# Kernel optimization log

Hardware: AMD Instinct MI355X
Metric: run time of the kernel (lower is better)

The kernel has to match this reference:

```python
import jax, jax.numpy as jnp
import numpy as np
import math

NUM_FILTERS = 128
SAMPLE_RATE = 16000
N_FFT = 2048
FREQ_MIN, FREQ_MAX = 20.0, 8000.0


def setup_inputs() -> dict:
    key = jax.random.key(0)
    B, FB, T = 32, N_FFT // 2 + 1, 2000
    spectrum = jax.random.normal(key, (B, FB, T), dtype=jnp.float32)
    # mel-scale init of center frequencies (in FFT-bin units), as in __init__
    mel_min = 2595.0 * math.log10(1.0 + FREQ_MIN / 700.0)
    mel_max = 2595.0 * math.log10(1.0 + FREQ_MAX / 700.0)
    mel_points = jnp.linspace(mel_min, mel_max, NUM_FILTERS, dtype=jnp.float32)
    freq_points = 700.0 * (10.0 ** (mel_points / 2595.0) - 1.0)
    center_freqs = freq_points * N_FFT / SAMPLE_RATE  # [F]
    bandwidths = jnp.full((NUM_FILTERS,), N_FFT / NUM_FILTERS / 4.0, dtype=jnp.float32)
    filter_shapes = jnp.ones((NUM_FILTERS, 2), dtype=jnp.float32)
    return {"spectrum": spectrum, "center_freqs": center_freqs,
            "bandwidths": bandwidths, "filter_shapes": filter_shapes}


def _build_filterbank(center_freqs, bandwidths, filter_shapes, freq_bins):
    # Vectorized over all filters: [F, freq_bins]
    freqs = jnp.arange(freq_bins, dtype=jnp.float32)[None, :]        # [1, K]
    center = center_freqs[:, None]                                    # [F, 1]
    bw = (jax.nn.softplus(bandwidths) + 0.001)[:, None]               # [F, 1]
    slopes = jax.nn.softplus(filter_shapes) + 0.1                     # [F, 2]
    left_edge = center - bw * slopes[:, 0:1]
    right_edge = center + bw * slopes[:, 1:2]
    rise = (freqs >= left_edge) & (freqs <= center)
    fall = (freqs > center) & (freqs <= right_edge)
    resp = jnp.where(rise, (freqs - left_edge) / (center - left_edge + 1e-8), 0.0)
    resp = jnp.where(fall, 1.0 - (freqs - center) / (right_edge - center + 1e-8), resp)
    return resp  # [F, K]


def reference(spectrum, center_freqs, bandwidths, filter_shapes):
    B, K, T = spectrum.shape
    F = center_freqs.shape[0]
    filterbank = _build_filterbank(center_freqs, bandwidths, filter_shapes, K)
    # [F, K] x [B, K, T] -> [B, F, T]
    filtered = jnp.einsum('fk,bkt->bft', filterbank, spectrum)
    # Faithful to original: reshape [B, F, T] -> [F, B, T], then permute(1,2,0) -> [B, T, F]
    filtered = filtered.reshape(F, B, T)
    return jnp.transpose(filtered, (1, 2, 0))
```

## Files before the change

### kernel.cpp

```cpp
#include <hip/hip_runtime.h>

#define K_BINS 1025
#define T_LEN  2000
#define NF     128
#define TQ     500

__device__ __forceinline__ float softplusf(float x) {
    return fmaxf(x, 0.0f) + log1pf(expf(-fabsf(x)));
}

__global__ __launch_bounds__(1024) void fb_fused(
        const float* __restrict__ spec,
        const float* __restrict__ cf,
        const float* __restrict__ bwv,
        const float* __restrict__ fs,
        float*       __restrict__ out) {
    const int q    = blockIdx.x;
    const int B    = blockIdx.y;
    const int th   = blockIdx.z;
    const int tid  = threadIdx.x;
    const int lane = tid & 63;
    const int wid  = tid >> 6;
    const int w    = wid >> 2;
    const int p    = wid & 3;
    const int bp   = 4 * q + p;
    const int t0   = TQ * th;

    float icl[4], irc[4], Af[4], Bf[4];
    int   klo[4], khi[4];
#pragma unroll
    for (int i = 0; i < 4; ++i) {
        const int f = 4 * B + 32 * w + i;
        float c  = cf[f];
        float bw = softplusf(bwv[f]) + 0.001f;
        float s0 = softplusf(fs[2 * f])     + 0.1f;
        float s1 = softplusf(fs[2 * f + 1]) + 0.1f;
        float left  = c - bw * s0;
        float right = c + bw * s1;
        icl[i] = 1.0f / (c - left + 1e-8f);
        irc[i] = 1.0f / (right - c + 1e-8f);
        Af[i]  = left * icl[i];
        Bf[i]  = fmaf(c, irc[i], 1.0f);
        klo[i] = max(0, (int)ceilf(left));
        khi[i] = min(K_BINS - 1, (int)floorf(right));
    }

    int rs[4], re[4], nr = 0;
    {
        int cs = klo[0], ce = khi[0];
#pragma unroll
        for (int i = 1; i < 4; ++i) {
            if (klo[i] <= ce + 1) ce = max(ce, khi[i]);
            else { rs[nr] = cs; re[nr] = ce; ++nr; cs = klo[i]; ce = khi[i]; }
        }
        rs[nr] = cs; re[nr] = ce; ++nr;
    }

    float4 acc[4][2];
#pragma unroll
    for (int i = 0; i < 4; ++i) {
        acc[i][0] = make_float4(0.f, 0.f, 0.f, 0.f);
        acc[i][1] = make_float4(0.f, 0.f, 0.f, 0.f);
    }

    const float4* base4 =
        (const float4*)(spec + (size_t)bp * (K_BINS * (size_t)T_LEN) + t0);
    const bool ok1 = (64 + lane) < (TQ / 4);

    int rcur = 0;
    int kcur = rs[0];
    float4 v0 = base4[(size_t)kcur * 500 + lane];
    float4 v1 = make_float4(0.f, 0.f, 0.f, 0.f);
    if (ok1) v1 = base4[(size_t)kcur * 500 + 64 + lane];

    while (kcur >= 0) {
        int knext, rnext = rcur;
        if (kcur + 1 <= re[rcur])      knext = kcur + 1;
        else if (rcur + 1 < nr)        { rnext = rcur + 1; knext = rs[rnext]; }
        else                           knext = -1;

        float4 n0, n1;
        if (knext >= 0) {
            const float4* np = base4 + (size_t)knext * 500;
            n0 = np[lane];
            if (ok1) n1 = np[64 + lane];
        }

        float fk = (float)kcur;
#pragma unroll
        for (int i = 0; i < 4; ++i) {
            float rise = fmaf(fk, icl[i], -Af[i]);
            float fall = fmaf(-fk, irc[i], Bf[i]);
            float wg   = fmaxf(0.0f, fminf(rise, fall));
            acc[i][0].x = fmaf(wg, v0.x, acc[i][0].x);
            acc[i][0].y = fmaf(wg, v0.y, acc[i][0].y);
            acc[i][0].z = fmaf(wg, v0.z, acc[i][0].z);
            acc[i][0].w = fmaf(wg, v0.w, acc[i][0].w);
            acc[i][1].x = fmaf(wg, v1.x, acc[i][1].x);
            acc[i][1].y = fmaf(wg, v1.y, acc[i][1].y);
            acc[i][1].z = fmaf(wg, v1.z, acc[i][1].z);
            acc[i][1].w = fmaf(wg, v1.w, acc[i][1].w);
        }
        v0 = n0; v1 = n1;
        kcur = knext; rcur = rnext;
    }

    __shared__ float tile[512][17];
#pragma unroll
    for (int i = 0; i < 4; ++i) {
        __syncthreads();
        {
            const int col = 4 * p + w;
            const int r0  = 4 * lane;
#pragma unroll
            for (int r = 0; r < 4; ++r)
                tile[r0 + r][col] = (&acc[i][0].x)[r];
            if (ok1) {
                const int r1 = 256 + 4 * lane;
#pragma unroll
                for (int r = 0; r < 4; ++r)
                    tile[r1 + r][col] = (&acc[i][1].x)[r];
            }
        }
        __syncthreads();
        const int b2 = 4 * B + i;
        const int c4 = tid & 3;
#pragma unroll
        for (int rr = 0; rr < 2; ++rr) {
            int tl = 256 * rr + (tid >> 2);
            if (tl < TQ) {
                float4 v = make_float4(tile[tl][4 * c4 + 0], tile[tl][4 * c4 + 1],
                                       tile[tl][4 * c4 + 2], tile[tl][4 * c4 + 3]);
                *reinterpret_cast<float4*>(
                    out + ((size_t)b2 * T_LEN + t0 + tl) * NF + 16 * q + 4 * c4) = v;
            }
        }
    }
}

extern "C" void kernel_launch(void* const* d_in, const int* in_sizes, int n_in,
                              void* d_out, int out_size, void* d_ws, size_t ws_size,
                              hipStream_t stream) {
    const float* spec = (const float*)d_in[0];
    const float* cf   = (const float*)d_in[1];
    const float* bwv  = (const float*)d_in[2];
    const float* fs   = (const float*)d_in[3];
    float* out = (float*)d_out;

    fb_fused<<<dim3(8, 8, 4), 1024, 0, stream>>>(spec, cf, bwv, fs, out);
}
```

Measured before the change: 61.91 us.

## Rebalance filter-band work per warp and narrow time tiles to one float4 per lane

Each warp now handles two filter groups, a band and its mirror (3-j, 7-Bp), so wide high-frequency filters pair with narrow low-frequency ones and per-warp k-loop lengths even out. The time axis is split into 8 tiles of 256 (last one 208), so each lane loads a single float4 per bin instead of two. The grid becomes 8x4x8 with the same block count. The aim is to cut the load imbalance across warps, where the slowest warp sets block time, at the cost of two sequential k-loops per warp and more output-tile passes through shared memory.

Result: slower. 69.07 us (+11.6%).

```diff
diff --git a/kernel.cpp b/kernel.cpp
--- a/kernel.cpp
+++ b/kernel.cpp
@@ -3,7 +3,6 @@
 #define K_BINS 1025
 #define T_LEN  2000
 #define NF     128
-#define TQ     500
 
 __device__ __forceinline__ float softplusf(float x) {
     return fmaxf(x, 0.0f) + log1pf(expf(-fabsf(x)));
@@ -16,123 +15,115 @@
         const float* __restrict__ fs,
         float*       __restrict__ out) {
     const int q    = blockIdx.x;
-    const int B    = blockIdx.y;
+    const int Bp   = blockIdx.y;
     const int th   = blockIdx.z;
     const int tid  = threadIdx.x;
     const int lane = tid & 63;
     const int wid  = tid >> 6;
-    const int w    = wid >> 2;
+    const int j    = wid >> 2;
     const int p    = wid & 3;
     const int bp   = 4 * q + p;
-    const int t0   = TQ * th;
-
-    float icl[4], irc[4], Af[4], Bf[4];
-    int   klo[4], khi[4];
-#pragma unroll
-    for (int i = 0; i < 4; ++i) {
-        const int f = 4 * B + 32 * w + i;
-        float c  = cf[f];
-        float bw = softplusf(bwv[f]) + 0.001f;
-        float s0 = softplusf(fs[2 * f])     + 0.1f;
-        float s1 = softplusf(fs[2 * f + 1]) + 0.1f;
-        float left  = c - bw * s0;
-        float right = c + bw * s1;
-        icl[i] = 1.0f / (c - left + 1e-8f);
-        irc[i] = 1.0f / (right - c + 1e-8f);
-        Af[i]  = left * icl[i];
-        Bf[i]  = fmaf(c, irc[i], 1.0f);
-        klo[i] = max(0, (int)ceilf(left));
-        khi[i] = min(K_BINS - 1, (int)floorf(right));
-    }
-
-    int rs[4], re[4], nr = 0;
-    {
-        int cs = klo[0], ce = khi[0];
-#pragma unroll
-        for (int i = 1; i < 4; ++i) {
-            if (klo[i] <= ce + 1) ce = max(ce, khi[i]);
-            else { rs[nr] = cs; re[nr] = ce; ++nr; cs = klo[i]; ce = khi[i]; }
-        }
-        rs[nr] = cs; re[nr] = ce; ++nr;
-    }
-
-    float4 acc[4][2];
-#pragma unroll
-    for (int i = 0; i < 4; ++i) {
-        acc[i][0] = make_float4(0.f, 0.f, 0.f, 0.f);
-        acc[i][1] = make_float4(0.f, 0.f, 0.f, 0.f);
-    }
+    const int t0   = 256 * th;
+    const int Lt   = (th < 7) ? 256 : 208;
+    const int Lq   = Lt >> 2;
+    const int li   = min(lane, Lq - 1);
 
     const float4* base4 =
         (const float4*)(spec + (size_t)bp * (K_BINS * (size_t)T_LEN) + t0);
-    const bool ok1 = (64 + lane) < (TQ / 4);
 
-    int rcur = 0;
-    int kcur = rs[0];
-    float4 v0 = base4[(size_t)kcur * 500 + lane];
-    float4 v1 = make_float4(0.f, 0.f, 0.f, 0.f);
-    if (ok1) v1 = base4[(size_t)kcur * 500 + 64 + lane];
+    float4 acc[2][4];
+#pragma unroll
+    for (int s = 0; s < 2; ++s)
+#pragma unroll
+        for (int i = 0; i < 4; ++i) acc[s][i] = make_float4(0.f, 0.f, 0.f, 0.f);
 
-    while (kcur >= 0) {
-        int knext, rnext = rcur;
-        if (kcur + 1 <= re[rcur])      knext = kcur + 1;
-        else if (rcur + 1 < nr)        { rnext = rcur + 1; knext = rs[rnext]; }
-        else                           knext = -1;
+#pragma unroll
+    for (int s = 0; s < 2; ++s) {
+        const int band  = s ? 3 - j : j;
+        const int Bq    = s ? 7 - Bp : Bp;
+        const int fbase = 4 * Bq + 32 * band;
 
-        float4 n0, n1;
-        if (knext >= 0) {
-            const float4* np = base4 + (size_t)knext * 500;
-            n0 = np[lane];
-            if (ok1) n1 = np[64 + lane];
+        float icl[4], irc[4], Af[4], Bf[4];
+        int   klo[4], khi[4];
+#pragma unroll
+        for (int i = 0; i < 4; ++i) {
+            const int f = fbase + i;
+            float c  = cf[f];
+            float bw = softplusf(bwv[f]) + 0.001f;
+            float s0 = softplusf(fs[2 * f])     + 0.1f;
+            float s1 = softplusf(fs[2 * f + 1]) + 0.1f;
+            float left  = c - bw * s0;
+            float right = c + bw * s1;
+            icl[i] = 1.0f / (c - left + 1e-8f);
+            irc[i] = 1.0f / (right - c + 1e-8f);
+            Af[i]  = left * icl[i];
+            Bf[i]  = fmaf(c, irc[i], 1.0f);
+            klo[i] = max(0, (int)ceilf(left));
+            khi[i] = min(K_BINS - 1, (int)floorf(right));
         }
 
-        float fk = (float)kcur;
+        int rs[4], re[4], nr = 0;
+        {
+            int cs = klo[0], ce = khi[0];
+#pragma unroll
+            for (int i = 1; i < 4; ++i) {
+                if (klo[i] <= ce + 1) ce = max(ce, khi[i]);
+                else { rs[nr] = cs; re[nr] = ce; ++nr; cs = klo[i]; ce = khi[i]; }
+            }
+            rs[nr] = cs; re[nr] = ce; ++nr;
+        }
+
+        int rcur = 0;
+        int kcur = rs[0];
+        float4 v = base4[(size_t)kcur * 500 + li];
+        while (kcur >= 0) {
+            int knext, rnext = rcur;
+            if (kcur + 1 <= re[rcur])      knext = kcur + 1;
+            else if (rcur + 1 < nr)        { rnext = rcur + 1; knext = rs[rnext]; }
+            else                           knext = -1;
+
+            float4 n;
+            if (knext >= 0) n = base4[(size_t)knext * 500 + li];
+
+            float fk = (float)kcur;
+#pragma unroll
+            for (int i = 0; i < 4; ++i) {
+                float rise = fmaf(fk, icl[i], -Af[i]);
+                float fall = fmaf(-fk, irc[i], Bf[i]);
+                float wg   = fmaxf(0.0f, fminf(rise, fall));
+                acc[s][i].x = fmaf(wg, v.x, acc[s][i].x);
+                acc[s][i].y = fmaf(wg, v.y, acc[s][i].y);
+                acc[s][i].z = fmaf(wg, v.z, acc[s][i].z);
+                acc[s][i].w = fmaf(wg, v.w, acc[s][i].w);
+            }
+            v = n; kcur = knext; rcur = rnext;
+        }
+    }
+
+    __shared__ float tile[256][17];
+#pragma unroll
+    for (int s = 0; s < 2; ++s) {
+        const int band = s ? 3 - j : j;
+        const int Bq   = s ? 7 - Bp : Bp;
+        const int col  = 4 * p + band;
 #pragma unroll
         for (int i = 0; i < 4; ++i) {
-            float rise = fmaf(fk, icl[i], -Af[i]);
-            float fall = fmaf(-fk, irc[i], Bf[i]);
-            float wg   = fmaxf(0.0f, fminf(rise, fall));
-            acc[i][0].x = fmaf(wg, v0.x, acc[i][0].x);
-            acc[i][0].y = fmaf(wg, v0.y, acc[i][0].y);
-            acc[i][0].z = fmaf(wg, v0.z, acc[i][0].z);
-            acc[i][0].w = fmaf(wg, v0.w, acc[i][0].w);
-            acc[i][1].x = fmaf(wg, v1.x, acc[i][1].x);
-            acc[i][1].y = fmaf(wg, v1.y, acc[i][1].y);
-            acc[i][1].z = fmaf(wg, v1.z, acc[i][1].z);
-            acc[i][1].w = fmaf(wg, v1.w, acc[i][1].w);
-        }
-        v0 = n0; v1 = n1;
-        kcur = knext; rcur = rnext;
-    }
-
-    __shared__ float tile[512][17];
-#pragma unroll
-    for (int i = 0; i < 4; ++i) {
-        __syncthreads();
-        {
-            const int col = 4 * p + w;
-            const int r0  = 4 * lane;
-#pragma unroll
-            for (int r = 0; r < 4; ++r)
-                tile[r0 + r][col] = (&acc[i][0].x)[r];
-            if (ok1) {
-                const int r1 = 256 + 4 * lane;
+            __syncthreads();
+            if (lane < Lq) {
+                const int rb = 4 * lane;
 #pragma unroll
                 for (int r = 0; r < 4; ++r)
-                    tile[r1 + r][col] = (&acc[i][1].x)[r];
+                    tile[rb + r][col] = (&acc[s][i].x)[r];
             }
-        }
-        __syncthreads();
-        const int b2 = 4 * B + i;
-        const int c4 = tid & 3;
-#pragma unroll
-        for (int rr = 0; rr < 2; ++rr) {
-            int tl = 256 * rr + (tid >> 2);
-            if (tl < TQ) {
-                float4 v = make_float4(tile[tl][4 * c4 + 0], tile[tl][4 * c4 + 1],
-                                       tile[tl][4 * c4 + 2], tile[tl][4 * c4 + 3]);
+            __syncthreads();
+            const int b2  = 4 * Bq + i;
+            const int row = tid >> 2;
+            const int c4  = tid & 3;
+            if (row < Lt) {
+                float4 v4 = make_float4(tile[row][4 * c4 + 0], tile[row][4 * c4 + 1],
+                                        tile[row][4 * c4 + 2], tile[row][4 * c4 + 3]);
                 *reinterpret_cast<float4*>(
-                    out + ((size_t)b2 * T_LEN + t0 + tl) * NF + 16 * q + 4 * c4) = v;
+                    out + ((size_t)b2 * T_LEN + t0 + row) * NF + 16 * q + 4 * c4) = v4;
             }
         }
     }
@@ -147,5 +138,5 @@
     const float* fs   = (const float*)d_in[3];
     float* out = (float*)d_out;
 
-    fb_fused<<<dim3(8, 8, 4), 1024, 0, stream>>>(spec, cf, bwv, fs, out);
+    fb_fused<<<dim3(8, 4, 8), 1024, 0, stream>>>(spec, cf, bwv, fs, out);
 }
```

## Fold four filter groups per wave and deepen row prefetch to three

Applied to the files above, without the earlier changes.

Blocks shrink from 1024 to 256 threads. Each wave now loops over four filter groups, which it previously shared with three other waves, and keeps all 4x4x2 float4 accumulators in registers. Inside each group, a three-slot rotating prefetch keeps several spectrum rows in flight ahead of the FMAs. The aim is more memory-level parallelism per wave, but register pressure rises sharply, occupancy per block drops, and the grid of 256 blocks leaves fewer waves in total to hide latency.

New measurement: 130.7 us. 2.11x slower.

```diff
diff --git a/kernel.cpp b/kernel.cpp
--- a/kernel.cpp
+++ b/kernel.cpp
@@ -4,12 +4,13 @@
 #define T_LEN  2000
 #define NF     128
 #define TQ     500
+#define ROWQ   500
 
 __device__ __forceinline__ float softplusf(float x) {
     return fmaxf(x, 0.0f) + log1pf(expf(-fabsf(x)));
 }
 
-__global__ __launch_bounds__(1024) void fb_fused(
+__global__ __launch_bounds__(256) void fb_fused(
         const float* __restrict__ spec,
         const float* __restrict__ cf,
         const float* __restrict__ bwv,
@@ -20,114 +21,132 @@
     const int th   = blockIdx.z;
     const int tid  = threadIdx.x;
     const int lane = tid & 63;
-    const int wid  = tid >> 6;
-    const int w    = wid >> 2;
-    const int p    = wid & 3;
+    const int p    = tid >> 6;
     const int bp   = 4 * q + p;
     const int t0   = TQ * th;
-
-    float icl[4], irc[4], Af[4], Bf[4];
-    int   klo[4], khi[4];
-#pragma unroll
-    for (int i = 0; i < 4; ++i) {
-        const int f = 4 * B + 32 * w + i;
-        float c  = cf[f];
-        float bw = softplusf(bwv[f]) + 0.001f;
-        float s0 = softplusf(fs[2 * f])     + 0.1f;
-        float s1 = softplusf(fs[2 * f + 1]) + 0.1f;
-        float left  = c - bw * s0;
-        float right = c + bw * s1;
-        icl[i] = 1.0f / (c - left + 1e-8f);
-        irc[i] = 1.0f / (right - c + 1e-8f);
-        Af[i]  = left * icl[i];
-        Bf[i]  = fmaf(c, irc[i], 1.0f);
-        klo[i] = max(0, (int)ceilf(left));
-        khi[i] = min(K_BINS - 1, (int)floorf(right));
-    }
-
-    int rs[4], re[4], nr = 0;
-    {
-        int cs = klo[0], ce = khi[0];
-#pragma unroll
-        for (int i = 1; i < 4; ++i) {
-            if (klo[i] <= ce + 1) ce = max(ce, khi[i]);
-            else { rs[nr] = cs; re[nr] = ce; ++nr; cs = klo[i]; ce = khi[i]; }
-        }
-        rs[nr] = cs; re[nr] = ce; ++nr;
-    }
-
-    float4 acc[4][2];
-#pragma unroll
-    for (int i = 0; i < 4; ++i) {
-        acc[i][0] = make_float4(0.f, 0.f, 0.f, 0.f);
-        acc[i][1] = make_float4(0.f, 0.f, 0.f, 0.f);
-    }
+    const bool ok1 = lane < (TQ / 4 - 64);
 
     const float4* base4 =
         (const float4*)(spec + (size_t)bp * (K_BINS * (size_t)T_LEN) + t0);
-    const bool ok1 = (64 + lane) < (TQ / 4);
 
-    int rcur = 0;
-    int kcur = rs[0];
-    float4 v0 = base4[(size_t)kcur * 500 + lane];
-    float4 v1 = make_float4(0.f, 0.f, 0.f, 0.f);
-    if (ok1) v1 = base4[(size_t)kcur * 500 + 64 + lane];
-
-    while (kcur >= 0) {
-        int knext, rnext = rcur;
-        if (kcur + 1 <= re[rcur])      knext = kcur + 1;
-        else if (rcur + 1 < nr)        { rnext = rcur + 1; knext = rs[rnext]; }
-        else                           knext = -1;
-
-        float4 n0, n1;
-        if (knext >= 0) {
-            const float4* np = base4 + (size_t)knext * 500;
-            n0 = np[lane];
-            if (ok1) n1 = np[64 + lane];
+    float4 acc[4][4][2];
+#pragma unroll
+    for (int w = 0; w < 4; ++w)
+#pragma unroll
+        for (int i = 0; i < 4; ++i) {
+            acc[w][i][0] = make_float4(0.f, 0.f, 0.f, 0.f);
+            acc[w][i][1] = make_float4(0.f, 0.f, 0.f, 0.f);
         }
 
-        float fk = (float)kcur;
+#pragma unroll
+    for (int w = 0; w < 4; ++w) {
+        float icl[4], mirc[4], mAf[4], Bf[4];
+        int   klo[4], khi[4];
 #pragma unroll
         for (int i = 0; i < 4; ++i) {
-            float rise = fmaf(fk, icl[i], -Af[i]);
-            float fall = fmaf(-fk, irc[i], Bf[i]);
-            float wg   = fmaxf(0.0f, fminf(rise, fall));
-            acc[i][0].x = fmaf(wg, v0.x, acc[i][0].x);
-            acc[i][0].y = fmaf(wg, v0.y, acc[i][0].y);
-            acc[i][0].z = fmaf(wg, v0.z, acc[i][0].z);
-            acc[i][0].w = fmaf(wg, v0.w, acc[i][0].w);
-            acc[i][1].x = fmaf(wg, v1.x, acc[i][1].x);
-            acc[i][1].y = fmaf(wg, v1.y, acc[i][1].y);
-            acc[i][1].z = fmaf(wg, v1.z, acc[i][1].z);
-            acc[i][1].w = fmaf(wg, v1.w, acc[i][1].w);
+            const int f = 4 * B + 32 * w + i;
+            float c  = cf[f];
+            float bw = softplusf(bwv[f]) + 0.001f;
+            float s0 = softplusf(fs[2 * f])     + 0.1f;
+            float s1 = softplusf(fs[2 * f + 1]) + 0.1f;
+            float left  = c - bw * s0;
+            float right = c + bw * s1;
+            float ic = 1.0f / (c - left + 1e-8f);
+            float ir = 1.0f / (right - c + 1e-8f);
+            icl[i]  = ic;
+            mirc[i] = -ir;
+            mAf[i]  = -left * ic;
+            Bf[i]   = fmaf(c, ir, 1.0f);
+            klo[i] = max(0, (int)ceilf(left));
+            khi[i] = min(K_BINS - 1, (int)floorf(right));
         }
-        v0 = n0; v1 = n1;
-        kcur = knext; rcur = rnext;
+
+        int rs[4], re[4], nr = 0;
+        {
+            int cs = klo[0], ce = khi[0];
+#pragma unroll
+            for (int i = 1; i < 4; ++i) {
+                if (klo[i] <= ce + 1) ce = max(ce, khi[i]);
+                else { rs[nr] = cs; re[nr] = ce; ++nr; cs = klo[i]; ce = khi[i]; }
+            }
+            rs[nr] = cs; re[nr] = ce; ++nr;
+        }
+
+        int rF = 0, kF = rs[0];
+        auto advance = [&]() {
+            if (kF + 1 <= re[rF]) ++kF;
+            else if (rF + 1 < nr) { ++rF; kF = rs[rF]; }
+            else kF = -1;
+        };
+
+#define LOADROW(d0, d1)                                                   \
+        { const float4* rp_ = base4 + (size_t)kF * ROWQ;                  \
+          d0 = rp_[lane]; if (ok1) d1 = rp_[64 + lane]; }
+
+#define COMPUTE(kk, v0, v1)                                               \
+        { float fk_ = (float)(kk);                                        \
+          _Pragma("unroll")                                               \
+          for (int i = 0; i < 4; ++i) {                                   \
+              float rise_ = fmaf(fk_, icl[i],  mAf[i]);                   \
+              float fall_ = fmaf(fk_, mirc[i], Bf[i]);                    \
+              float wg_   = fmaxf(0.0f, fminf(rise_, fall_));             \
+              acc[w][i][0].x = fmaf(wg_, v0.x, acc[w][i][0].x);           \
+              acc[w][i][0].y = fmaf(wg_, v0.y, acc[w][i][0].y);           \
+              acc[w][i][0].z = fmaf(wg_, v0.z, acc[w][i][0].z);           \
+              acc[w][i][0].w = fmaf(wg_, v0.w, acc[w][i][0].w);           \
+              acc[w][i][1].x = fmaf(wg_, v1.x, acc[w][i][1].x);           \
+              acc[w][i][1].y = fmaf(wg_, v1.y, acc[w][i][1].y);           \
+              acc[w][i][1].z = fmaf(wg_, v1.z, acc[w][i][1].z);           \
+              acc[w][i][1].w = fmaf(wg_, v1.w, acc[w][i][1].w);           \
+          } }
+
+#define STEP(S0, S1, KS)                                                  \
+        { float4 n0_, n1_; int nk_ = -1;                                  \
+          if (kF >= 0) { LOADROW(n0_, n1_); nk_ = kF; advance(); }        \
+          COMPUTE(KS, S0, S1);                                            \
+          S0 = n0_; S1 = n1_; KS = nk_; }
+
+        float4 A0, A1, Bv0, Bv1, C0, C1;
+        int kA = -1, kB = -1, kC = -1;
+        if (kF >= 0) { LOADROW(A0, A1);   kA = kF; advance(); }
+        if (kF >= 0) { LOADROW(Bv0, Bv1); kB = kF; advance(); }
+        if (kF >= 0) { LOADROW(C0, C1);   kC = kF; advance(); }
+
+        while (kA >= 0) {
+            STEP(A0, A1, kA);
+            if (kB < 0) break;
+            STEP(Bv0, Bv1, kB);
+            if (kC < 0) break;
+            STEP(C0, C1, kC);
+        }
+#undef STEP
+#undef COMPUTE
+#undef LOADROW
     }
 
     __shared__ float tile[512][17];
 #pragma unroll
     for (int i = 0; i < 4; ++i) {
         __syncthreads();
-        {
+#pragma unroll
+        for (int w = 0; w < 4; ++w) {
             const int col = 4 * p + w;
-            const int r0  = 4 * lane;
+            const int rb  = 4 * lane;
 #pragma unroll
             for (int r = 0; r < 4; ++r)
-                tile[r0 + r][col] = (&acc[i][0].x)[r];
+                tile[rb + r][col] = (&acc[w][i][0].x)[r];
             if (ok1) {
-                const int r1 = 256 + 4 * lane;
 #pragma unroll
                 for (int r = 0; r < 4; ++r)
-                    tile[r1 + r][col] = (&acc[i][1].x)[r];
+                    tile[256 + rb + r][col] = (&acc[w][i][1].x)[r];
             }
         }
         __syncthreads();
         const int b2 = 4 * B + i;
         const int c4 = tid & 3;
 #pragma unroll
-        for (int rr = 0; rr < 2; ++rr) {
-            int tl = 256 * rr + (tid >> 2);
+        for (int rr = 0; rr < 8; ++rr) {
+            int tl = 64 * rr + (tid >> 2);
             if (tl < TQ) {
                 float4 v = make_float4(tile[tl][4 * c4 + 0], tile[tl][4 * c4 + 1],
                                        tile[tl][4 * c4 + 2], tile[tl][4 * c4 + 3]);
@@ -147,5 +166,5 @@
     const float* fs   = (const float*)d_in[3];
     float* out = (float*)d_out;
 
-    fb_fused<<<dim3(8, 8, 4), 1024, 0, stream>>>(spec, cf, bwv, fs, out);
+    fb_fused<<<dim3(8, 8, 4), 256, 0, stream>>>(spec, cf, bwv, fs, out);
 }
```
